# Kernel optimization log

Measured on AMD Instinct MI355X. Metric: run time of the kernel, lower is better.

Reference implementation:

```python
import jax, jax.numpy as jnp
import numpy as np

K = 3  # de_neighbors
NUM_STAGES = 4


def _square_distance(a, b):
    # a: [B,N,3], b: [B,S,3] -> [B,N,S] squared euclidean distances
    return (jnp.sum(a * a, -1)[:, :, None]
            + jnp.sum(b * b, -1)[:, None, :]
            - 2.0 * jnp.einsum('bnd,bsd->bns', a, b))


def _propagate(xyz1, xyz2, points1, points2, k):
    # xyz1: [B,N,3] fine coords; xyz2: [B,S,3] coarse coords
    # points1: [B,C1,N] skip feats (or None); points2: [B,C2,S] coarse feats
    p2 = jnp.transpose(points2, (0, 2, 1))  # [B,S,C2]
    N = xyz1.shape[1]
    S = xyz2.shape[1]
    if S == 1:
        interp = jnp.tile(p2, (1, N, 1))
    else:
        d = _square_distance(xyz1, xyz2)            # [B,N,S]
        neg_d, idx = jax.lax.top_k(-d, k)           # k smallest dists
        dk = -neg_d                                 # [B,N,k]
        w = 1.0 / (dk + 1e-8)
        w = w / jnp.sum(w, axis=-1, keepdims=True)  # [B,N,k]
        gathered = jax.vmap(lambda p, i: p[i])(p2, idx)  # [B,N,k,C2]
        interp = jnp.sum(gathered * w[..., None], axis=2)  # [B,N,C2]
    if points1 is not None:
        interp = jnp.concatenate([jnp.transpose(points1, (0, 2, 1)), interp], axis=-1)
    return jnp.transpose(interp, (0, 2, 1))  # [B,C1+C2,N]


def setup_inputs() -> dict:
    key = jax.random.key(0)
    ks = jax.random.split(key, 10)
    B = 16
    Ns = [4096, 1024, 256, 64, 16]
    Cs = [64, 128, 256, 512, 1024]
    out = {}
    for i in range(5):
        out[f'xyz{i}'] = jax.random.normal(ks[i], (B, Ns[i], 3), dtype=jnp.float32)
        out[f'f{i}'] = jax.random.normal(ks[5 + i], (B, Cs[i], Ns[i]), dtype=jnp.float32)
    return out


def reference(xyz0, xyz1, xyz2, xyz3, xyz4, f0, f1, f2, f3, f4):
    # forward() reverses the fine->coarse lists to coarse->fine
    xyz = [xyz4, xyz3, xyz2, xyz1, xyz0]
    feats = [f4, f3, f2, f1, f0]
    x = feats[0]
    for i in range(NUM_STAGES):
        x = _propagate(xyz[i + 1], xyz[i], feats[i + 1], x, K)
    return x  # [B, 1984, 4096]
```

## Files before the change

### kernel.cpp

```cpp
#include <hip/hip_runtime.h>

#define B 16
typedef float f32x4 __attribute__((ext_vector_type(4)));

__global__ __launch_bounds__(256) void knn_all_kernel(
    const float* __restrict__ xyz0, const float* __restrict__ xyz1,
    const float* __restrict__ xyz2, const float* __restrict__ xyz3,
    const float* __restrict__ xyz4,
    int4* idx0, float4* w0, int4* idx1, float4* w1,
    int4* idx2, float4* w2, int4* idx3, float4* w3) {
    __shared__ float lds[(256 + 1) * 4 * 4];
    int bid = blockIdx.x;
    int S, logS4;
    const float *xf, *xc;
    int4* io; float4* wo;
    if (bid < 1024)      { S = 1024; logS4 = 8; xf = xyz0; xc = xyz1; io = idx3; wo = w3; }
    else if (bid < 1280) { bid -= 1024; S = 256; logS4 = 6; xf = xyz1; xc = xyz2; io = idx2; wo = w2; }
    else if (bid < 1344) { bid -= 1280; S = 64;  logS4 = 4; xf = xyz2; xc = xyz3; io = idx1; wo = w1; }
    else                 { bid -= 1344; S = 16;  logS4 = 2; xf = xyz3; xc = xyz4; io = idx0; wo = w0; }
    const int N = S << 2;
    const int lognb = logS4 - 2;
    const int b = bid >> lognb;
    const int nblk = bid & ((1 << lognb) - 1);
    const int S4 = S >> 2;

    const float* cbase = xc + (size_t)b * S * 3;
    for (int j = threadIdx.x; j < S; j += 256) {
        float x = cbase[j * 3 + 0], y = cbase[j * 3 + 1], z = cbase[j * 3 + 2];
        int seg = j >> logS4, jj = j & (S4 - 1);
        float* p = lds + (size_t)(seg * (S4 + 1) + jj) * 4;
        p[0] = x; p[1] = y; p[2] = z; p[3] = x * x + y * y + z * z;
    }
    __syncthreads();
    const int t = threadIdx.x;
    const int sub = t & 3;
    const int n = nblk * 64 + (t >> 2);
    const float* fp = xf + ((size_t)b * N + n) * 3;
    const float ax = fp[0], ay = fp[1], az = fp[2];
    const float an2 = ax * ax + ay * ay + az * az;
    float d0 = 1e30f, d1 = 1e30f, d2 = 1e30f;
    int i0 = -1, i1 = -1, i2 = -1;
    const f32x4* seg4 = reinterpret_cast<const f32x4*>(lds) + sub * (S4 + 1);
    const int jbase = sub * S4;
#pragma unroll 4
    for (int k = 0; k < S4; ++k) {
        f32x4 c = seg4[k];
        float d = an2 + c[3] - 2.0f * (ax * c[0] + ay * c[1] + az * c[2]);
        int j = jbase + k;
        if (d < d2) {
            if (d < d1) {
                d2 = d1; i2 = i1;
                if (d < d0) { d1 = d0; i1 = i0; d0 = d; i0 = j; }
                else        { d1 = d;  i1 = j; }
            } else { d2 = d; i2 = j; }
        }
    }
#pragma unroll
    for (int r = 1; r <= 2; r <<= 1) {
        float e0 = __shfl_xor(d0, r), e1 = __shfl_xor(d1, r), e2 = __shfl_xor(d2, r);
        int   j0 = __shfl_xor(i0, r), j1 = __shfl_xor(i1, r), j2 = __shfl_xor(i2, r);
        float ed[3] = {e0, e1, e2};
        int   ej[3] = {j0, j1, j2};
#pragma unroll
        for (int m = 0; m < 3; ++m) {
            float d = ed[m]; int j = ej[m];
            if (d < d0 || (d == d0 && j < i0)) {
                d2 = d1; i2 = i1; d1 = d0; i1 = i0; d0 = d; i0 = j;
            } else if (d < d1 || (d == d1 && j < i1)) {
                d2 = d1; i2 = i1; d1 = d; i1 = j;
            } else if (d < d2 || (d == d2 && j < i2)) {
                d2 = d; i2 = j;
            }
        }
    }
    if (sub == 0) {
        float w0_ = 1.0f / (d0 + 1e-8f);
        float w1_ = 1.0f / (d1 + 1e-8f);
        float w2_ = 1.0f / (d2 + 1e-8f);
        float inv = 1.0f / (w0_ + w1_ + w2_);
        size_t o = (size_t)b * N + n;
        io[o] = make_int4(i0, i1, i2, 0);
        wo[o] = make_float4(w0_ * inv, w1_ * inv, w2_ * inv, 0.0f);
    }
}


template <int P>
__device__ __forceinline__ void copy_planes(const float* __restrict__ src_rows,
                                            f32x4* dst, int t) {
    constexpr int P4 = P / 4;
    const f32x4* src = reinterpret_cast<const f32x4*>(src_rows);
    float* df = reinterpret_cast<float*>(dst);
    for (int e = t; e < 8 * P4; e += 256) {
        int c = e / P4;
        int s4 = e & (P4 - 1);
        f32x4 v = src[c * P4 + s4];
        int base = (((c >> 2) * P + s4 * 4) << 2) + (c & 3);
        df[base + 0] = v[0]; df[base + 4] = v[1];
        df[base + 8] = v[2]; df[base + 12] = v[3];
    }
}

template <int PD, int PS>
__device__ __forceinline__ void expand(const f32x4* src, f32x4* dst,
                                       const int4* __restrict__ idxL,
                                       const f32x4* __restrict__ wL,
                                       int b, int t) {
    for (int e = t; e < 2 * PD; e += 256) {
        int p = (e >= PD) ? 1 : 0;
        int s = e - p * PD;
        int4 id = idxL[(size_t)b * PD + s];
        f32x4 ww = wL[(size_t)b * PD + s];
        const f32x4* sp = src + p * PS;
        dst[e] = ww[0] * sp[id.x] + ww[1] * sp[id.y] + ww[2] * sp[id.z];
    }
}

__global__ __launch_bounds__(256) void decode_kernel(
    const float* __restrict__ f0, const float* __restrict__ f1,
    const float* __restrict__ f2, const float* __restrict__ f3,
    const float* __restrict__ f4,
    const int4* __restrict__ idx0, const f32x4* __restrict__ w0,
    const int4* __restrict__ idx1, const f32x4* __restrict__ w1,
    const int4* __restrict__ idx2, const f32x4* __restrict__ w2,
    const int4* __restrict__ idx3, const f32x4* __restrict__ w3,
    float* __restrict__ out) {
    __shared__ f32x4 s3[2 * 1024];
    __shared__ f32x4 s2[2 * 256];
    __shared__ f32x4 s1[2 * 64];
    __shared__ f32x4 s0[2 * 16];
    const int b = blockIdx.x;
    const int c0 = blockIdx.y * 8;
    const int t = threadIdx.x;
    float* outb = out + ((size_t)b * 1984 + c0) * 4096;

    if (c0 < 64) {
        const f32x4* src = reinterpret_cast<const f32x4*>(f0 + ((size_t)b * 64 + c0) * 4096);
        f32x4* dst = reinterpret_cast<f32x4*>(outb);
        for (int i = t; i < 8 * 1024; i += 256) dst[i] = src[i];
        return;
    }
    const int cx = c0 - 64;
    if (cx < 128) {
        copy_planes<1024>(f1 + ((size_t)b * 128 + cx) * 1024, s3, t);
        __syncthreads();
    } else if (cx < 384) {
        copy_planes<256>(f2 + ((size_t)b * 256 + (cx - 128)) * 256, s2, t);
        __syncthreads();
        expand<1024, 256>(s2, s3, idx2, w2, b, t);
        __syncthreads();
    } else if (cx < 896) {
        copy_planes<64>(f3 + ((size_t)b * 512 + (cx - 384)) * 64, s1, t);
        __syncthreads();
        expand<256, 64>(s1, s2, idx1, w1, b, t);
        __syncthreads();
        expand<1024, 256>(s2, s3, idx2, w2, b, t);
        __syncthreads();
    } else {
        copy_planes<16>(f4 + ((size_t)b * 1024 + (cx - 896)) * 16, s0, t);
        __syncthreads();
        expand<64, 16>(s0, s1, idx0, w0, b, t);
        __syncthreads();
        expand<256, 64>(s1, s2, idx1, w1, b, t);
        __syncthreads();
        expand<1024, 256>(s2, s3, idx2, w2, b, t);
        __syncthreads();
    }
    const int4* idxF = idx3 + (size_t)b * 4096;
    const f32x4* wF = w3 + (size_t)b * 4096;
    for (int it = 0; it < 4; ++it) {
        const int n0 = (it * 256 + t) * 4;
        int4 id[4]; f32x4 ww[4];
#pragma unroll
        for (int q = 0; q < 4; ++q) { id[q] = idxF[n0 + q]; ww[q] = wF[n0 + q]; }
#pragma unroll
        for (int p = 0; p < 2; ++p) {
            const f32x4* pl = s3 + p * 1024;
            f32x4 v[4];
#pragma unroll
            for (int q = 0; q < 4; ++q) {
                v[q] = ww[q][0] * pl[id[q].x] + ww[q][1] * pl[id[q].y]
                     + ww[q][2] * pl[id[q].z];
            }
            float* ob = outb + (size_t)(p * 4) * 4096 + n0;
#pragma unroll
            for (int j = 0; j < 4; ++j) {
                f32x4 st = {v[0][j], v[1][j], v[2][j], v[3][j]};
                *reinterpret_cast<f32x4*>(ob + (size_t)j * 4096) = st;
            }
        }
    }
}

extern "C" void kernel_launch(void* const* d_in, const int* in_sizes, int n_in,
                              void* d_out, int out_size, void* d_ws, size_t ws_size,
                              hipStream_t stream) {
    static const int xyzSz[5] = {16 * 4096 * 3, 16 * 1024 * 3, 16 * 256 * 3,
                                 16 * 64 * 3, 16 * 16 * 3};
    static const int fSz[5] = {16 * 64 * 4096, 16 * 128 * 1024, 16 * 256 * 256,
                               16 * 512 * 64, 16 * 1024 * 16};
    const float* xyz[5] = {nullptr, nullptr, nullptr, nullptr, nullptr};
    const float* f[5] = {nullptr, nullptr, nullptr, nullptr, nullptr};
    for (int i = 0; i < n_in; ++i) {
        for (int j = 0; j < 5; ++j) {
            if (in_sizes[i] == xyzSz[j] && !xyz[j]) { xyz[j] = (const float*)d_in[i]; goto next; }
            if (in_sizes[i] == fSz[j] && !f[j])     { f[j] = (const float*)d_in[i];  goto next; }
        }
    next:;
    }

    char* ws = (char*)d_ws;
    int4*   idx3 = (int4*)(ws);
    float4* w3   = (float4*)(ws + (1u << 20));
    int4*   idx2 = (int4*)(ws + (2u << 20));
    float4* w2   = (float4*)(ws + (2u << 20) + 262144u);
    int4*   idx1 = (int4*)(ws + (2u << 20) + 524288u);
    float4* w1   = (float4*)(ws + (2u << 20) + 589824u);
    int4*   idx0 = (int4*)(ws + (2u << 20) + 655360u);
    float4* w0   = (float4*)(ws + (2u << 20) + 671744u);

    knn_all_kernel<<<1360, 256, 0, stream>>>(
        xyz[0], xyz[1], xyz[2], xyz[3], xyz[4],
        idx0, w0, idx1, w1, idx2, w2, idx3, w3);

    decode_kernel<<<dim3(B, 248), 256, 0, stream>>>(
        f[0], f[1], f[2], f[3], f[4],
        idx0, (const f32x4*)w0, idx1, (const f32x4*)w1,
        idx2, (const f32x4*)w2, idx3, (const f32x4*)w3,
        (float*)d_out);
}
```

Before: 150.6 us.

## Move f0 passthrough copy into knn kernel, alias LDS buffers, use nontemporal stores

The f0 skip-feature copy moves out of the decode kernel into 128 extra blocks of the knn kernel, so the bandwidth-bound copy overlaps the compute-bound kNN search. The decode kernel's LDS planes are aliased into one smaller buffer to raise occupancy. Its blocks are issued in reverse channel order so the deepest (longest) expansion chains start first. Output writes use nontemporal stores and the final loop is partially unrolled. The risk is that the extra copy blocks slow the knn phase, and that the aliased buffers must never be live at the same time.

```diff
diff --git a/kernel.cpp b/kernel.cpp
--- a/kernel.cpp
+++ b/kernel.cpp
@@ -6,11 +6,23 @@
 __global__ __launch_bounds__(256) void knn_all_kernel(
     const float* __restrict__ xyz0, const float* __restrict__ xyz1,
     const float* __restrict__ xyz2, const float* __restrict__ xyz3,
-    const float* __restrict__ xyz4,
+    const float* __restrict__ xyz4, const float* __restrict__ f0,
+    float* __restrict__ out,
     int4* idx0, float4* w0, int4* idx1, float4* w1,
     int4* idx2, float4* w2, int4* idx3, float4* w3) {
     __shared__ float lds[(256 + 1) * 4 * 4];
     int bid = blockIdx.x;
+    if (bid >= 1360) {
+        bid -= 1360;
+        const int b = bid >> 3;
+        const int c0 = (bid & 7) * 8;
+        const f32x4* src = reinterpret_cast<const f32x4*>(f0 + ((size_t)b * 64 + c0) * 4096);
+        f32x4* dst = reinterpret_cast<f32x4*>(out + ((size_t)b * 1984 + c0) * 4096);
+        for (int i = threadIdx.x; i < 8 * 1024; i += 256) {
+            __builtin_nontemporal_store(__builtin_nontemporal_load(src + i), dst + i);
+        }
+        return;
+    }
     int S, logS4;
     const float *xf, *xc;
     int4* io; float4* wo;
@@ -117,30 +129,23 @@
 }
 
 __global__ __launch_bounds__(256) void decode_kernel(
-    const float* __restrict__ f0, const float* __restrict__ f1,
-    const float* __restrict__ f2, const float* __restrict__ f3,
-    const float* __restrict__ f4,
+    const float* __restrict__ f1, const float* __restrict__ f2,
+    const float* __restrict__ f3, const float* __restrict__ f4,
     const int4* __restrict__ idx0, const f32x4* __restrict__ w0,
     const int4* __restrict__ idx1, const f32x4* __restrict__ w1,
     const int4* __restrict__ idx2, const f32x4* __restrict__ w2,
     const int4* __restrict__ idx3, const f32x4* __restrict__ w3,
     float* __restrict__ out) {
-    __shared__ f32x4 s3[2 * 1024];
-    __shared__ f32x4 s2[2 * 256];
-    __shared__ f32x4 s1[2 * 64];
-    __shared__ f32x4 s0[2 * 16];
+    __shared__ f32x4 buf[2560];
+    f32x4* s3 = buf;
+    f32x4* s2 = buf + 2048;
+    f32x4* s1 = buf;
+    f32x4* s0 = buf + 128;
     const int b = blockIdx.x;
-    const int c0 = blockIdx.y * 8;
+    const int cx = (239 - blockIdx.y) * 8;
     const int t = threadIdx.x;
-    float* outb = out + ((size_t)b * 1984 + c0) * 4096;
-
-    if (c0 < 64) {
-        const f32x4* src = reinterpret_cast<const f32x4*>(f0 + ((size_t)b * 64 + c0) * 4096);
-        f32x4* dst = reinterpret_cast<f32x4*>(outb);
-        for (int i = t; i < 8 * 1024; i += 256) dst[i] = src[i];
-        return;
-    }
-    const int cx = c0 - 64;
+    float* outb = out + ((size_t)b * 1984 + 64 + cx) * 4096;
+
     if (cx < 128) {
         copy_planes<1024>(f1 + ((size_t)b * 128 + cx) * 1024, s3, t);
         __syncthreads();
@@ -168,6 +173,7 @@
     }
     const int4* idxF = idx3 + (size_t)b * 4096;
     const f32x4* wF = w3 + (size_t)b * 4096;
+#pragma unroll 2
     for (int it = 0; it < 4; ++it) {
         const int n0 = (it * 256 + t) * 4;
         int4 id[4]; f32x4 ww[4];
@@ -186,7 +192,7 @@
 #pragma unroll
             for (int j = 0; j < 4; ++j) {
                 f32x4 st = {v[0][j], v[1][j], v[2][j], v[3][j]};
-                *reinterpret_cast<f32x4*>(ob + (size_t)j * 4096) = st;
+                __builtin_nontemporal_store(st, reinterpret_cast<f32x4*>(ob + (size_t)j * 4096));
             }
         }
     }
@@ -219,12 +225,12 @@
     int4*   idx0 = (int4*)(ws + (2u << 20) + 655360u);
     float4* w0   = (float4*)(ws + (2u << 20) + 671744u);
 
-    knn_all_kernel<<<1360, 256, 0, stream>>>(
-        xyz[0], xyz[1], xyz[2], xyz[3], xyz[4],
+    knn_all_kernel<<<1488, 256, 0, stream>>>(
+        xyz[0], xyz[1], xyz[2], xyz[3], xyz[4], f[0], (float*)d_out,
         idx0, w0, idx1, w1, idx2, w2, idx3, w3);
 
-    decode_kernel<<<dim3(B, 248), 256, 0, stream>>>(
-        f[0], f[1], f[2], f[3], f[4],
+    decode_kernel<<<dim3(B, 240), 256, 0, stream>>>(
+        f[1], f[2], f[3], f[4],
         idx0, (const f32x4*)w0, idx1, (const f32x4*)w1,
         idx2, (const f32x4*)w2, idx3, (const f32x4*)w3,
         (float*)d_out);
```

After: 130.4 us, median of 2. 13.4% less time.
